# Kernel tuning notes

Hardware: AMD Instinct MI355X
Metric: run time of the kernel (lower is better)

Reference implementation:

```python
import jax, jax.numpy as jnp
import numpy as np

T = 0.1          # temperature from module
NORM_EPS = 1e-12 # F.normalize default eps
COS_EPS = 1e-6   # nn.CosineSimilarity eps

def setup_inputs() -> dict:
    key = jax.random.key(0)
    k1, k2, k3 = jax.random.split(key, 3)
    B, D = 8192, 2048
    return {
        "embed": jax.random.normal(k1, (B, D), dtype=jnp.float32),
        "embed_enhance": jax.random.normal(k2, (B, D), dtype=jnp.float32),
        "labels": jax.random.uniform(k3, (B,), dtype=jnp.float32),
    }

def reference(embed, embed_enhance, labels):
    # Faithful to the original module, INCLUDING the early `return loss`
    # inside the `for i` loop: only i == 0 contributes.
    labels = labels.astype(jnp.float32)
    B = embed.shape[0]
    # F.normalize(embed, dim=-1)
    en = embed / jnp.maximum(jnp.linalg.norm(embed, axis=-1, keepdims=True), NORM_EPS)
    a = en[0]                                                # [D], normalized anchor
    na = jnp.maximum(jnp.linalg.norm(a), COS_EPS)
    nb = jnp.maximum(jnp.linalg.norm(embed_enhance, axis=-1), COS_EPS)  # [B]
    cos = (embed_enhance @ a) / (na * nb)                    # [B] cosine sims vs row 0
    mask = jnp.arange(B) != 0                                # exclude j == i == 0
    neg = -cos / T                                           # = log(exp(-cos/t))
    E0 = 1e-12 + jnp.sum(jnp.where(mask, jnp.exp(neg), 0.0))
    C0 = 1e-12 + jnp.sum(jnp.where(mask, labels[0] * labels, 0.0))
    Cij = labels[0] * labels / C0                            # [B]
    L0 = jnp.sum(jnp.where(mask, -Cij * (neg - jnp.log(E0)), 0.0))
    return L0 / B
```

## Files before the change

### kernel.cpp

```cpp
#include <hip/hip_runtime.h>
#include <math.h>

static constexpr int Dn = 2048;
static constexpr int Bn = 8192;

__device__ __forceinline__ float dot4(float4 a, float4 b) {
    return a.x * b.x + a.y * b.y + a.z * b.z + a.w * b.w;
}

__global__ __launch_bounds__(256) void k_anchor(const float* __restrict__ embed,
                                                float* __restrict__ a_out,
                                                float* __restrict__ na_out) {
    __shared__ float red[8];
    const int t = threadIdx.x;
    const int lane = t & 63, wave = t >> 6;

    float4 v0 = reinterpret_cast<const float4*>(embed)[t];
    float4 v1 = reinterpret_cast<const float4*>(embed)[t + 256];

    float ss = dot4(v0, v0) + dot4(v1, v1);
#pragma unroll
    for (int o = 32; o > 0; o >>= 1) ss += __shfl_down(ss, o, 64);
    if (lane == 0) red[wave] = ss;
    __syncthreads();
    if (t == 0) red[4] = red[0] + red[1] + red[2] + red[3];
    __syncthreads();

    const float inv = 1.0f / fmaxf(sqrtf(red[4]), 1e-12f);
    float4 a0, a1;
    a0.x = v0.x * inv; a0.y = v0.y * inv; a0.z = v0.z * inv; a0.w = v0.w * inv;
    a1.x = v1.x * inv; a1.y = v1.y * inv; a1.z = v1.z * inv; a1.w = v1.w * inv;
    reinterpret_cast<float4*>(a_out)[t]       = a0;
    reinterpret_cast<float4*>(a_out)[t + 256] = a1;

    float ssa = dot4(a0, a0) + dot4(a1, a1);
#pragma unroll
    for (int o = 32; o > 0; o >>= 1) ssa += __shfl_down(ssa, o, 64);
    __syncthreads();
    if (lane == 0) red[wave] = ssa;
    __syncthreads();
    if (t == 0) *na_out = fmaxf(sqrtf(red[0] + red[1] + red[2] + red[3]), 1e-6f);
}

__global__ __launch_bounds__(256) void k_rows(const float* __restrict__ ee,
                                              const float* __restrict__ a,
                                              const float* __restrict__ na_p,
                                              float* __restrict__ neg_out) {
    __shared__ float rd[4], rs[4];
    const int t = threadIdx.x;
    const int lane = t & 63, wave = t >> 6;
    const int j = blockIdx.x;

    const float4* row = reinterpret_cast<const float4*>(ee + (size_t)j * Dn);
    const float4* av  = reinterpret_cast<const float4*>(a);

    float4 e0 = row[t], e1 = row[t + 256];
    float4 a0 = av[t],  a1 = av[t + 256];

    float dot = dot4(e0, a0) + dot4(e1, a1);
    float ss  = dot4(e0, e0) + dot4(e1, e1);
#pragma unroll
    for (int o = 32; o > 0; o >>= 1) {
        dot += __shfl_down(dot, o, 64);
        ss  += __shfl_down(ss,  o, 64);
    }
    if (lane == 0) { rd[wave] = dot; rs[wave] = ss; }
    __syncthreads();
    if (t == 0) {
        const float dtot = rd[0] + rd[1] + rd[2] + rd[3];
        const float stot = rs[0] + rs[1] + rs[2] + rs[3];
        const float nb   = fmaxf(sqrtf(stot), 1e-6f);
        const float cosv = dtot / ((*na_p) * nb);
        neg_out[j] = -cosv * 10.0f;
    }
}

__global__ __launch_bounds__(256) void k_final(const float* __restrict__ neg,
                                               const float* __restrict__ labels,
                                               float* __restrict__ out) {
    __shared__ double rE[4], rL[4], rN[4];
    const int t = threadIdx.x;
    const int lane = t & 63, wave = t >> 6;

    double sE = 0.0, sL = 0.0, sN = 0.0;
    for (int j = t; j < Bn; j += 256) {
        if (j == 0) continue;
        const float ng = neg[j];
        const float lb = labels[j];
        sE += (double)expf(ng);
        sL += (double)lb;
        sN += (double)lb * (double)ng;
    }
#pragma unroll
    for (int o = 32; o > 0; o >>= 1) {
        sE += __shfl_down(sE, o, 64);
        sL += __shfl_down(sL, o, 64);
        sN += __shfl_down(sN, o, 64);
    }
    if (lane == 0) { rE[wave] = sE; rL[wave] = sL; rN[wave] = sN; }
    __syncthreads();
    if (t == 0) {
        const double E0 = 1e-12 + rE[0] + rE[1] + rE[2] + rE[3];
        const double S2 = rL[0] + rL[1] + rL[2] + rL[3];
        const double S3 = rN[0] + rN[1] + rN[2] + rN[3];
        const double l0 = (double)labels[0];
        const double C0 = 1e-12 + l0 * S2;
        const double L0 = -(l0 / C0) * (S3 - log(E0) * S2);
        out[0] = (float)(L0 / (double)Bn);
    }
}

extern "C" void kernel_launch(void* const* d_in, const int* in_sizes, int n_in,
                              void* d_out, int out_size, void* d_ws, size_t ws_size,
                              hipStream_t stream) {
    const float* embed  = (const float*)d_in[0];
    const float* ee     = (const float*)d_in[1];
    const float* labels = (const float*)d_in[2];
    float* out = (float*)d_out;

    float* ws  = (float*)d_ws;
    float* a   = ws;
    float* na  = ws + 2048;
    float* neg = ws + 2560;

    k_anchor<<<1, 256, 0, stream>>>(embed, a, na);
    k_rows<<<Bn, 256, 0, stream>>>(ee, a, na, neg);
    k_final<<<1, 256, 0, stream>>>(neg, labels, out);
}
```

Baseline: 139.0 us.

## Fuse anchor normalization and row dot products into one wave-per-row kernel

```diff
diff --git a/kernel.cpp b/kernel.cpp
--- a/kernel.cpp
+++ b/kernel.cpp
@@ -3,79 +3,75 @@
 
 static constexpr int Dn = 2048;
 static constexpr int Bn = 8192;
+static constexpr int NBLK  = 1024;
+static constexpr int NWAVE = NBLK * 4;
 
 __device__ __forceinline__ float dot4(float4 a, float4 b) {
     return a.x * b.x + a.y * b.y + a.z * b.z + a.w * b.w;
 }
 
-__global__ __launch_bounds__(256) void k_anchor(const float* __restrict__ embed,
-                                                float* __restrict__ a_out,
-                                                float* __restrict__ na_out) {
-    __shared__ float red[8];
-    const int t = threadIdx.x;
-    const int lane = t & 63, wave = t >> 6;
+__global__ __launch_bounds__(256) void k_main(const float* __restrict__ embed,
+                                              const float* __restrict__ ee,
+                                              const float* __restrict__ labels,
+                                              double* __restrict__ part) {
+    const int t    = threadIdx.x;
+    const int lane = t & 63;
+    const int wv   = ((int)blockIdx.x << 2) | (t >> 6);
 
-    float4 v0 = reinterpret_cast<const float4*>(embed)[t];
-    float4 v1 = reinterpret_cast<const float4*>(embed)[t + 256];
+    const float4* e0 = reinterpret_cast<const float4*>(embed);
+    float4 av[8];
+    float ss = 0.f;
+#pragma unroll
+    for (int s = 0; s < 8; ++s) {
+        av[s] = e0[(s << 6) + lane];
+        ss += dot4(av[s], av[s]);
+    }
+#pragma unroll
+    for (int o = 32; o > 0; o >>= 1) ss += __shfl_xor(ss, o, 64);
+    const float inv = 1.0f / fmaxf(sqrtf(ss), 1e-12f);
 
-    float ss = dot4(v0, v0) + dot4(v1, v1);
+    float ssa = 0.f;
 #pragma unroll
-    for (int o = 32; o > 0; o >>= 1) ss += __shfl_down(ss, o, 64);
-    if (lane == 0) red[wave] = ss;
-    __syncthreads();
-    if (t == 0) red[4] = red[0] + red[1] + red[2] + red[3];
-    __syncthreads();
+    for (int s = 0; s < 8; ++s) {
+        av[s].x *= inv; av[s].y *= inv; av[s].z *= inv; av[s].w *= inv;
+        ssa += dot4(av[s], av[s]);
+    }
+#pragma unroll
+    for (int o = 32; o > 0; o >>= 1) ssa += __shfl_xor(ssa, o, 64);
+    const float na = fmaxf(sqrtf(ssa), 1e-6f);
 
-    const float inv = 1.0f / fmaxf(sqrtf(red[4]), 1e-12f);
-    float4 a0, a1;
-    a0.x = v0.x * inv; a0.y = v0.y * inv; a0.z = v0.z * inv; a0.w = v0.w * inv;
-    a1.x = v1.x * inv; a1.y = v1.y * inv; a1.z = v1.z * inv; a1.w = v1.w * inv;
-    reinterpret_cast<float4*>(a_out)[t]       = a0;
-    reinterpret_cast<float4*>(a_out)[t + 256] = a1;
-
-    float ssa = dot4(a0, a0) + dot4(a1, a1);
+    double sE = 0.0, sL = 0.0, sN = 0.0;
+    for (int j = wv; j < Bn; j += NWAVE) {
+        const float4* row = reinterpret_cast<const float4*>(ee + (size_t)j * Dn);
+        float dt = 0.f, sr = 0.f;
 #pragma unroll
-    for (int o = 32; o > 0; o >>= 1) ssa += __shfl_down(ssa, o, 64);
-    __syncthreads();
-    if (lane == 0) red[wave] = ssa;
-    __syncthreads();
-    if (t == 0) *na_out = fmaxf(sqrtf(red[0] + red[1] + red[2] + red[3]), 1e-6f);
-}
-
-__global__ __launch_bounds__(256) void k_rows(const float* __restrict__ ee,
-                                              const float* __restrict__ a,
-                                              const float* __restrict__ na_p,
-                                              float* __restrict__ neg_out) {
-    __shared__ float rd[4], rs[4];
-    const int t = threadIdx.x;
-    const int lane = t & 63, wave = t >> 6;
-    const int j = blockIdx.x;
-
-    const float4* row = reinterpret_cast<const float4*>(ee + (size_t)j * Dn);
-    const float4* av  = reinterpret_cast<const float4*>(a);
-
-    float4 e0 = row[t], e1 = row[t + 256];
-    float4 a0 = av[t],  a1 = av[t + 256];
-
-    float dot = dot4(e0, a0) + dot4(e1, a1);
-    float ss  = dot4(e0, e0) + dot4(e1, e1);
+        for (int s = 0; s < 8; ++s) {
+            const float4 r = row[(s << 6) + lane];
+            dt += dot4(r, av[s]);
+            sr += dot4(r, r);
+        }
 #pragma unroll
-    for (int o = 32; o > 0; o >>= 1) {
-        dot += __shfl_down(dot, o, 64);
-        ss  += __shfl_down(ss,  o, 64);
+        for (int o = 32; o > 0; o >>= 1) {
+            dt += __shfl_xor(dt, o, 64);
+            sr += __shfl_xor(sr, o, 64);
+        }
+        if (lane == 0 && j != 0) {
+            const float nb  = fmaxf(sqrtf(sr), 1e-6f);
+            const float neg = -10.0f * dt / (na * nb);
+            const double lb = (double)labels[j];
+            sE += (double)expf(neg);
+            sL += lb;
+            sN += lb * (double)neg;
+        }
     }
-    if (lane == 0) { rd[wave] = dot; rs[wave] = ss; }
-    __syncthreads();
-    if (t == 0) {
-        const float dtot = rd[0] + rd[1] + rd[2] + rd[3];
-        const float stot = rs[0] + rs[1] + rs[2] + rs[3];
-        const float nb   = fmaxf(sqrtf(stot), 1e-6f);
-        const float cosv = dtot / ((*na_p) * nb);
-        neg_out[j] = -cosv * 10.0f;
+    if (lane == 0) {
+        part[wv]             = sE;
+        part[NWAVE + wv]     = sL;
+        part[2 * NWAVE + wv] = sN;
     }
 }
 
-__global__ __launch_bounds__(256) void k_final(const float* __restrict__ neg,
+__global__ __launch_bounds__(256) void k_final(const double* __restrict__ part,
                                                const float* __restrict__ labels,
                                                float* __restrict__ out) {
     __shared__ double rE[4], rL[4], rN[4];
@@ -83,13 +79,10 @@
     const int lane = t & 63, wave = t >> 6;
 
     double sE = 0.0, sL = 0.0, sN = 0.0;
-    for (int j = t; j < Bn; j += 256) {
-        if (j == 0) continue;
-        const float ng = neg[j];
-        const float lb = labels[j];
-        sE += (double)expf(ng);
-        sL += (double)lb;
-        sN += (double)lb * (double)ng;
+    for (int i = t; i < NWAVE; i += 256) {
+        sE += part[i];
+        sL += part[NWAVE + i];
+        sN += part[2 * NWAVE + i];
     }
 #pragma unroll
     for (int o = 32; o > 0; o >>= 1) {
@@ -118,12 +111,8 @@
     const float* labels = (const float*)d_in[2];
     float* out = (float*)d_out;
 
-    float* ws  = (float*)d_ws;
-    float* a   = ws;
-    float* na  = ws + 2048;
-    float* neg = ws + 2560;
+    double* part = (double*)d_ws;
 
-    k_anchor<<<1, 256, 0, stream>>>(embed, a, na);
-    k_rows<<<Bn, 256, 0, stream>>>(ee, a, na, neg);
-    k_final<<<1, 256, 0, stream>>>(neg, labels, out);
+    k_main<<<NBLK, 256, 0, stream>>>(embed, ee, labels, part);
+    k_final<<<1, 256, 0, stream>>>(part, labels, out);
 }
```

After: 128.4 us. 7.7% less time.
